# Performance work log

Measured on AMD Instinct MI355X. Metric: run time of the kernel, lower is better.

The kernel has to match this reference:

```python
import jax, jax.numpy as jnp
import numpy as np

B, S, D, K, N = 4, 4096, 768, 24, 8192

def setup_inputs() -> dict:
    key = jax.random.key(0)
    k1, k2, k3, k4 = jax.random.split(key, 4)
    x = jax.random.normal(k1, (B, S, D), dtype=jnp.float32)
    phi = jax.random.normal(k2, (S, K), dtype=jnp.float32)
    M_inputs = jax.random.normal(k3, (D, D), dtype=jnp.float32) / np.sqrt(D)
    M_filters = jax.random.normal(k4, (K, D), dtype=jnp.float32) / np.sqrt(K)
    return {"x": x, "phi": phi, "M_inputs": M_inputs, "M_filters": M_filters, "n": N}


def reference(x, phi, M_inputs, M_filters, n):
    # STU.forward with use_approx=True, use_flash_fft=False
    bsz, sl, d = x.shape
    x_proj = x @ M_inputs               # [B, S, D]
    phi_proj = phi @ M_filters          # [S, D]
    # alternating sign sequence for the 'minus' spectral branch
    sgn = jnp.ones((1, sl, 1), dtype=x.dtype).at[:, 1::2].set(-1.0)
    # filters: [1, S, D, 1] broadcast over the plus/minus stack
    v = phi_proj[None, :, :, None]
    V = jnp.fft.rfft(v, n=n, axis=1)    # [1, n//2+1, D, 1] complex
    U = jnp.stack([x_proj, x_proj * sgn], axis=-1)  # [B, S, D, 2]
    Uf = jnp.fft.rfft(U, n=n, axis=1)   # [B, n//2+1, D, 2]
    U_conv = jnp.fft.irfft(V * Uf, n=n, axis=1)[:, :sl]  # [B, S, D, 2]
    spectral_plus = U_conv[..., 0]
    spectral_minus = U_conv[..., 1] * sgn
    return spectral_plus + spectral_minus
```

## Files before the change

kernel.cpp:

```cpp
#include <hip/hip_runtime.h>
#include <hip/hip_bf16.h>


#define NB 4
#define NS 4096
#define ND 768
#define NK 24

typedef __attribute__((ext_vector_type(8))) short short8;
typedef __attribute__((ext_vector_type(4))) float f32x4;
typedef __attribute__((ext_vector_type(4))) unsigned short u16x4;

static __device__ __forceinline__ float bf2f(unsigned short u) {
  union { unsigned int i; float f; } v; v.i = ((unsigned int)u) << 16; return v.f;
}
static __device__ __forceinline__ unsigned short f2bf(float f) {
  union { float f; unsigned int i; } v; v.f = f;
  return (unsigned short)((v.i + 0x7fffu + ((v.i >> 16) & 1u)) >> 16);
}

__device__ __forceinline__ float2 cadd(float2 a, float2 b){ return make_float2(a.x+b.x, a.y+b.y); }
__device__ __forceinline__ float2 csub(float2 a, float2 b){ return make_float2(a.x-b.x, a.y-b.y); }
__device__ __forceinline__ float2 cmul(float2 a, float2 b){ return make_float2(a.x*b.x-a.y*b.y, a.x*b.y+a.y*b.x); }

#define C4 0.70710678118654752f
#define C8 0.92387953251128674f
#define S8 0.38268343236508977f
#define TWO_PI 6.28318530717958648f

__device__ __forceinline__ void fft16_dif(float2 v[16]) {
  const float twr[8] = {1.f, C8, C4, S8, 0.f, -S8, -C4, -C8};
  const float twi[8] = {0.f, -S8, -C4, -C8, -1.f, -C8, -C4, -S8};
#pragma unroll
  for (int i = 0; i < 8; ++i) {
    float2 a = v[i], b = v[i+8];
    v[i] = cadd(a, b);
    float2 d = csub(a, b);
    v[i+8] = make_float2(d.x*twr[i]-d.y*twi[i], d.x*twi[i]+d.y*twr[i]);
  }
#pragma unroll
  for (int blk = 0; blk < 16; blk += 8)
#pragma unroll
    for (int i = 0; i < 4; ++i) {
      float2 a = v[blk+i], b = v[blk+i+4];
      v[blk+i] = cadd(a, b);
      float2 d = csub(a, b);
      v[blk+i+4] = make_float2(d.x*twr[2*i]-d.y*twi[2*i], d.x*twi[2*i]+d.y*twr[2*i]);
    }
#pragma unroll
  for (int blk = 0; blk < 16; blk += 4) {
    { float2 a = v[blk],   b = v[blk+2]; v[blk] = cadd(a,b);   v[blk+2] = csub(a,b); }
    { float2 a = v[blk+1], b = v[blk+3]; float2 d = csub(a,b);
      v[blk+1] = cadd(a,b); v[blk+3] = make_float2(d.y, -d.x); }
  }
#pragma unroll
  for (int blk = 0; blk < 16; blk += 2) {
    float2 a = v[blk], b = v[blk+1];
    v[blk] = cadd(a, b); v[blk+1] = csub(a, b);
  }
}

__device__ __forceinline__ void idft16(float2 v[16]) {
  const float twr[8] = {1.f, C8, C4, S8, 0.f, -S8, -C4, -C8};
  const float twi[8] = {0.f, S8, C4, C8, 1.f, C8, C4, S8};
#pragma unroll
  for (int blk = 0; blk < 16; blk += 2) {
    float2 a = v[blk], b = v[blk+1];
    v[blk] = cadd(a, b); v[blk+1] = csub(a, b);
  }
#pragma unroll
  for (int blk = 0; blk < 16; blk += 4) {
    { float2 a = v[blk],   b = v[blk+2]; v[blk] = cadd(a,b);   v[blk+2] = csub(a,b); }
    { float2 a = v[blk+1], b = v[blk+3]; float2 t = make_float2(-b.y, b.x);
      v[blk+1] = cadd(a,t); v[blk+3] = csub(a,t); }
  }
#pragma unroll
  for (int blk = 0; blk < 16; blk += 8)
#pragma unroll
    for (int i = 0; i < 4; ++i) {
      float2 b = v[blk+i+4];
      float2 t = make_float2(b.x*twr[2*i]-b.y*twi[2*i], b.x*twi[2*i]+b.y*twr[2*i]);
      float2 a = v[blk+i];
      v[blk+i] = cadd(a, t); v[blk+i+4] = csub(a, t);
    }
#pragma unroll
  for (int i = 0; i < 8; ++i) {
    float2 b = v[i+8];
    float2 t = make_float2(b.x*twr[i]-b.y*twi[i], b.x*twi[i]+b.y*twr[i]);
    float2 a = v[i];
    v[i] = cadd(a, t); v[i+8] = csub(a, t);
  }
}

#define BR_TABLE {0,8,4,12,2,10,6,14,1,9,5,13,3,11,7,15}
#define PAD(i) ((i) + ((i) >> 4))

__global__ __launch_bounds__(256) void cast_x_bf16(const float* __restrict__ in,
                                                   unsigned short* __restrict__ out) {
  int i = (blockIdx.x * 256 + threadIdx.x) * 4;
  float4 v = *(const float4*)(in + i);
  u16x4 o = { f2bf(v.x), f2bf(v.y), f2bf(v.z), f2bf(v.w) };
  *(u16x4*)(out + i) = o;
}

__global__ __launch_bounds__(256) void transpose_cast_Mi(const float* __restrict__ Mi,
                                                         unsigned short* __restrict__ MiT) {
  int idx = blockIdx.x * 256 + threadIdx.x;
  int d = idx / ND, e = idx % ND;
  MiT[idx] = f2bf(Mi[e * ND + d]);
}

__global__ __launch_bounds__(256) void phi_proj_kernel(const float* __restrict__ phi,
                                                       const float* __restrict__ Mf,
                                                       float* __restrict__ phiE) {
  int d = blockIdx.y;
  int m = blockIdx.x * 256 + threadIdx.x;
  int s = 2 * m;
  float acc = 0.f;
#pragma unroll
  for (int k = 0; k < NK; ++k) acc += phi[s * NK + k] * Mf[k * ND + d];
  phiE[d * 2048 + m] = acc;
}

__global__ __launch_bounds__(256) void gemm_xprojT(const unsigned short* __restrict__ Xb,
                                                   const unsigned short* __restrict__ MiT,
                                                   unsigned short* __restrict__ XPT) {
  __shared__ unsigned short As[128 * 32];
  __shared__ unsigned short Bs[128 * 32];
  const int tid = threadIdx.x;
  const int r0 = blockIdx.x * 128;
  const int c0 = blockIdx.y * 128;
  const int lane = tid & 63;
  const int wave = tid >> 6;
  const int wr = (wave >> 1) * 64;
  const int wc = (wave & 1) * 64;

  f32x4 acc[4][4];
#pragma unroll
  for (int m = 0; m < 4; ++m)
#pragma unroll
    for (int n = 0; n < 4; ++n) acc[m][n] = (f32x4){0.f, 0.f, 0.f, 0.f};

  for (int k0 = 0; k0 < ND; k0 += 32) {
    short8 va[2], vb[2];
#pragma unroll
    for (int i = 0; i < 2; ++i) {
      int slot = tid + 256 * i;
      int row = slot >> 2, kc = slot & 3;
      va[i] = *(const short8*)(Xb + (size_t)(r0 + row) * ND + k0 + kc * 8);
      vb[i] = *(const short8*)(MiT + (size_t)(c0 + row) * ND + k0 + kc * 8);
    }
    __syncthreads();
#pragma unroll
    for (int i = 0; i < 2; ++i) {
      int slot = tid + 256 * i;
      *(short8*)(As + slot * 8) = va[i];
      *(short8*)(Bs + slot * 8) = vb[i];
    }
    __syncthreads();

    short8 a[4], b[4];
#pragma unroll
    for (int m = 0; m < 4; ++m)
      a[m] = *(const short8*)(As + (wr + m * 16 + (lane & 15)) * 32 + (lane >> 4) * 8);
#pragma unroll
    for (int n = 0; n < 4; ++n)
      b[n] = *(const short8*)(Bs + (wc + n * 16 + (lane & 15)) * 32 + (lane >> 4) * 8);
#pragma unroll
    for (int m = 0; m < 4; ++m)
#pragma unroll
      for (int n = 0; n < 4; ++n)
        acc[m][n] = __builtin_amdgcn_mfma_f32_16x16x32_bf16(a[m], b[n], acc[m][n], 0, 0, 0);
  }

  const int bI = r0 >> 12;
  const int sBase = r0 & (NS - 1);
#pragma unroll
  for (int m = 0; m < 4; ++m) {
#pragma unroll
    for (int n = 0; n < 4; ++n) {
      int col = c0 + wc + n * 16 + (lane & 15);
      int srow = sBase + wr + m * 16 + (lane >> 4) * 4;
      f32x4 v = acc[m][n];
      u16x4 o = { f2bf(v[0]), f2bf(v[1]), f2bf(v[2]), f2bf(v[3]) };
      *(u16x4*)(XPT + ((size_t)bI * ND + col) * NS + srow) = o;
    }
  }
}

__global__ __launch_bounds__(256) void filter_fft(const float* __restrict__ phiE,
                                                  float2* __restrict__ Hbr) {
  __shared__ float LR[4352], LI[4352];
  const int d = blockIdx.x;
  const int tid = threadIdx.x;
  const int BR[16] = BR_TABLE;
  float2 v[16];
  const float* src = phiE + (size_t)d * 2048;
#pragma unroll
  for (int n2 = 0; n2 < 16; ++n2)
    v[n2] = (n2 < 8) ? make_float2(src[n2 * 256 + tid], 0.f) : make_float2(0.f, 0.f);

  float sn, cs;
  fft16_dif(v);
  __sincosf(-(TWO_PI / 4096.f) * (float)tid, &sn, &cs);
  { float2 step = make_float2(cs, sn), w = make_float2(1.f, 0.f);
#pragma unroll
    for (int p = 1; p < 16; ++p) { w = cmul(w, step); v[BR[p]] = cmul(v[BR[p]], w); } }
#pragma unroll
  for (int r = 0; r < 16; ++r) { int i = BR[r] * 256 + tid; int s = PAD(i); LR[s] = v[r].x; LI[s] = v[r].y; }
  __syncthreads();

  const int p2 = tid >> 4, n0 = tid & 15;
#pragma unroll
  for (int n1 = 0; n1 < 16; ++n1) { int i = p2 * 256 + n1 * 16 + n0; int s = PAD(i); v[n1] = make_float2(LR[s], LI[s]); }
  fft16_dif(v);
  __sincosf(-(TWO_PI / 256.f) * (float)n0, &sn, &cs);
  { float2 step = make_float2(cs, sn), w = make_float2(1.f, 0.f);
#pragma unroll
    for (int p = 1; p < 16; ++p) { w = cmul(w, step); v[BR[p]] = cmul(v[BR[p]], w); } }
  __syncthreads();
#pragma unroll
  for (int r = 0; r < 16; ++r) { int i = p2 * 256 + BR[r] * 16 + n0; int s = PAD(i); LR[s] = v[r].x; LI[s] = v[r].y; }
  __syncthreads();

#pragma unroll
  for (int q = 0; q < 16; ++q) { int i = tid * 16 + q; int s = PAD(i); v[q] = make_float2(LR[s], LI[s]); }
  fft16_dif(v);
  const float sc = 2.0f / 4096.0f;
  float2* H = Hbr + (size_t)d * 4096;
#pragma unroll
  for (int r = 0; r < 16; ++r)
    H[r * 256 + tid] = make_float2(v[r].x * sc, v[r].y * sc);
}

__global__ __launch_bounds__(256) void conv_kernel(const unsigned short* __restrict__ XPT,
                                                   const float2* __restrict__ Hbr,
                                                   float* __restrict__ outT) {
  __shared__ float LR[4352], LI[4352];
  const int bd = blockIdx.x;
  const int d = bd % ND;
  const int tid = threadIdx.x;
  const int BR[16] = BR_TABLE;
  float2 v[16];
  float sn, cs;

  const unsigned int* src = (const unsigned int*)(XPT + (size_t)bd * NS);
#pragma unroll
  for (int n2 = 0; n2 < 16; ++n2) {
    if (n2 < 8) {
      unsigned int w = src[n2 * 256 + tid];
      v[n2] = make_float2(bf2f((unsigned short)(w & 0xffffu)), bf2f((unsigned short)(w >> 16)));
    } else v[n2] = make_float2(0.f, 0.f);
  }

  fft16_dif(v);
  __sincosf(-(TWO_PI / 4096.f) * (float)tid, &sn, &cs);
  { float2 step = make_float2(cs, sn), w = make_float2(1.f, 0.f);
#pragma unroll
    for (int p = 1; p < 16; ++p) { w = cmul(w, step); v[BR[p]] = cmul(v[BR[p]], w); } }
#pragma unroll
  for (int r = 0; r < 16; ++r) { int i = BR[r] * 256 + tid; int s = PAD(i); LR[s] = v[r].x; LI[s] = v[r].y; }
  __syncthreads();

  const int p2 = tid >> 4, n0 = tid & 15;
#pragma unroll
  for (int n1 = 0; n1 < 16; ++n1) { int i = p2 * 256 + n1 * 16 + n0; int s = PAD(i); v[n1] = make_float2(LR[s], LI[s]); }
  fft16_dif(v);
  __sincosf(-(TWO_PI / 256.f) * (float)n0, &sn, &cs);
  { float2 step = make_float2(cs, sn), w = make_float2(1.f, 0.f);
#pragma unroll
    for (int p = 1; p < 16; ++p) { w = cmul(w, step); v[BR[p]] = cmul(v[BR[p]], w); } }
  __syncthreads();
#pragma unroll
  for (int r = 0; r < 16; ++r) { int i = p2 * 256 + BR[r] * 16 + n0; int s = PAD(i); LR[s] = v[r].x; LI[s] = v[r].y; }
  __syncthreads();

#pragma unroll
  for (int q = 0; q < 16; ++q) { int i = tid * 16 + q; int s = PAD(i); v[q] = make_float2(LR[s], LI[s]); }
  fft16_dif(v);
  const float2* H = Hbr + (size_t)d * 4096;
#pragma unroll
  for (int r = 0; r < 16; ++r) v[r] = cmul(v[r], H[r * 256 + tid]);
  idft16(v);
  __sincosf((TWO_PI / 256.f) * (float)(tid & 15), &sn, &cs);
  { float2 step = make_float2(cs, sn), w = make_float2(1.f, 0.f);
#pragma unroll
    for (int n = 1; n < 16; ++n) { w = cmul(w, step); v[n] = cmul(v[n], w); } }
#pragma unroll
  for (int n = 0; n < 16; ++n) { int i = tid * 16 + n; int s = PAD(i); LR[s] = v[n].x; LI[s] = v[n].y; }
  __syncthreads();

#pragma unroll
  for (int r = 0; r < 16; ++r) { int i = p2 * 256 + BR[r] * 16 + n0; int s = PAD(i); v[r] = make_float2(LR[s], LI[s]); }
  idft16(v);
  {
    float sn0, cs0;
    __sincosf((TWO_PI / 4096.f) * (float)(n0 * p2), &sn0, &cs0);
    __sincosf((TWO_PI / 256.f) * (float)p2, &sn, &cs);
    float2 step = make_float2(cs, sn), w = make_float2(cs0, sn0);
    v[0] = cmul(v[0], w);
#pragma unroll
    for (int n = 1; n < 16; ++n) { w = cmul(w, step); v[n] = cmul(v[n], w); }
  }
  __syncthreads();
#pragma unroll
  for (int n = 0; n < 16; ++n) { int i = p2 * 256 + n * 16 + n0; int s = PAD(i); LR[s] = v[n].x; LI[s] = v[n].y; }
  __syncthreads();

#pragma unroll
  for (int r = 0; r < 16; ++r) { int i = BR[r] * 256 + tid; int s = PAD(i); v[r] = make_float2(LR[s], LI[s]); }
  idft16(v);
  float* dst = outT + (size_t)bd * NS;
#pragma unroll
  for (int n2 = 0; n2 < 8; ++n2)
    *(float2*)(dst + ((n2 << 8) + tid) * 2) = v[n2];
}

__global__ __launch_bounds__(256) void transpose_out(const float* __restrict__ outT,
                                                     float* __restrict__ out) {
  __shared__ float tile[64][65];
  const int b = blockIdx.z;
  const int d0 = blockIdx.y * 64;
  const int s0 = blockIdx.x * 64;
  const int tid = threadIdx.x;
#pragma unroll
  for (int i = 0; i < 16; ++i) {
    int dd = (tid >> 6) + i * 4;
    int ss = tid & 63;
    tile[dd][ss] = outT[((size_t)b * ND + d0 + dd) * NS + s0 + ss];
  }
  __syncthreads();
#pragma unroll
  for (int i = 0; i < 16; ++i) {
    int ss = (tid >> 6) + i * 4;
    int dd = tid & 63;
    out[((size_t)b * NS + s0 + ss) * ND + d0 + dd] = tile[dd][ss];
  }
}

extern "C" void kernel_launch(void* const* d_in, const int* in_sizes, int n_in,
                              void* d_out, int out_size, void* d_ws, size_t ws_size,
                              hipStream_t stream) {
  const float* x   = (const float*)d_in[0];
  const float* phi = (const float*)d_in[1];
  const float* Mi  = (const float*)d_in[2];
  const float* Mf  = (const float*)d_in[3];
  float* out = (float*)d_out;

  const size_t SZ_XPT = (size_t)NB * ND * NS * 2;
  const size_t SZ_HBR = (size_t)ND * 4096 * 8;
  const size_t SZ_POOL = (size_t)NB * ND * NS * 4;
  if (ws_size < SZ_XPT + SZ_HBR + SZ_POOL) return;

  char* ws = (char*)d_ws;
  unsigned short* xprojT = (unsigned short*)ws;
  float2* Hbr = (float2*)(ws + SZ_XPT);
  char* pool = ws + SZ_XPT + SZ_HBR;
  unsigned short* xbf = (unsigned short*)pool;
  unsigned short* MiT = (unsigned short*)(pool + 25165824);
  float* phiE = (float*)(pool + 25165824 + 1179648);
  float* outT = (float*)pool;

  cast_x_bf16<<<(NB * NS * ND) / (256 * 4), 256, 0, stream>>>(x, xbf);
  transpose_cast_Mi<<<(ND * ND) / 256, 256, 0, stream>>>(Mi, MiT);
  phi_proj_kernel<<<dim3(2048 / 256, ND), 256, 0, stream>>>(phi, Mf, phiE);
  gemm_xprojT<<<dim3((NB * NS) / 128, ND / 128), 256, 0, stream>>>(xbf, MiT, xprojT);
  filter_fft<<<ND, 256, 0, stream>>>(phiE, Hbr);
  conv_kernel<<<NB * ND, 256, 0, stream>>>(xprojT, Hbr, outT);
  transpose_out<<<dim3(NS / 64, ND / 64, NB), 256, 0, stream>>>(outT, out);
}
```

Measured before the change: 136.7 us.

## Table twiddles, prune zero-padded FFT stages, bf16 intermediate, direct-to-LDS GEMM loads

Bundles several changes. A precomputed twiddle table replaces per-thread sincos and chained complex multiplies. Specialised FFT stages skip the zero-padded half on input and the unused half on output. The phi projection is fused into filter_fft, the Mi transpose is tiled through LDS, and the GEMM uses global_load_lds with a swapped grid order. The conv output is stored as bf16 to halve transpose traffic, at the cost of extra rounding error in the final result.

Result: slower. 175.1 us (+28.1%).

```diff
diff --git a/kernel.cpp b/kernel.cpp
--- a/kernel.cpp
+++ b/kernel.cpp
@@ -22,6 +22,7 @@
 __device__ __forceinline__ float2 cadd(float2 a, float2 b){ return make_float2(a.x+b.x, a.y+b.y); }
 __device__ __forceinline__ float2 csub(float2 a, float2 b){ return make_float2(a.x-b.x, a.y-b.y); }
 __device__ __forceinline__ float2 cmul(float2 a, float2 b){ return make_float2(a.x*b.x-a.y*b.y, a.x*b.y+a.y*b.x); }
+__device__ __forceinline__ float2 cmulc(float2 a, float2 b){ return make_float2(a.x*b.x+a.y*b.y, a.y*b.x-a.x*b.y); }
 
 #define C4 0.70710678118654752f
 #define C8 0.92387953251128674f
@@ -60,6 +61,37 @@
   }
 }
 
+__device__ __forceinline__ void fft16_dif_zero8(float2 v[16]) {
+  const float twr[8] = {1.f, C8, C4, S8, 0.f, -S8, -C4, -C8};
+  const float twi[8] = {0.f, -S8, -C4, -C8, -1.f, -C8, -C4, -S8};
+#pragma unroll
+  for (int i = 1; i < 8; ++i) {
+    float2 a = v[i];
+    v[i+8] = make_float2(a.x*twr[i]-a.y*twi[i], a.x*twi[i]+a.y*twr[i]);
+  }
+  v[8] = v[0];
+#pragma unroll
+  for (int blk = 0; blk < 16; blk += 8)
+#pragma unroll
+    for (int i = 0; i < 4; ++i) {
+      float2 a = v[blk+i], b = v[blk+i+4];
+      v[blk+i] = cadd(a, b);
+      float2 d = csub(a, b);
+      v[blk+i+4] = make_float2(d.x*twr[2*i]-d.y*twi[2*i], d.x*twi[2*i]+d.y*twr[2*i]);
+    }
+#pragma unroll
+  for (int blk = 0; blk < 16; blk += 4) {
+    { float2 a = v[blk],   b = v[blk+2]; v[blk] = cadd(a,b);   v[blk+2] = csub(a,b); }
+    { float2 a = v[blk+1], b = v[blk+3]; float2 d = csub(a,b);
+      v[blk+1] = cadd(a,b); v[blk+3] = make_float2(d.y, -d.x); }
+  }
+#pragma unroll
+  for (int blk = 0; blk < 16; blk += 2) {
+    float2 a = v[blk], b = v[blk+1];
+    v[blk] = cadd(a, b); v[blk+1] = csub(a, b);
+  }
+}
+
 __device__ __forceinline__ void idft16(float2 v[16]) {
   const float twr[8] = {1.f, C8, C4, S8, 0.f, -S8, -C4, -C8};
   const float twi[8] = {0.f, S8, C4, C8, 1.f, C8, C4, S8};
@@ -92,8 +124,48 @@
   }
 }
 
+__device__ __forceinline__ void idft16_low8(float2 v[16]) {
+  const float twr[8] = {1.f, C8, C4, S8, 0.f, -S8, -C4, -C8};
+  const float twi[8] = {0.f, S8, C4, C8, 1.f, C8, C4, S8};
+#pragma unroll
+  for (int blk = 0; blk < 16; blk += 2) {
+    float2 a = v[blk], b = v[blk+1];
+    v[blk] = cadd(a, b); v[blk+1] = csub(a, b);
+  }
+#pragma unroll
+  for (int blk = 0; blk < 16; blk += 4) {
+    { float2 a = v[blk],   b = v[blk+2]; v[blk] = cadd(a,b);   v[blk+2] = csub(a,b); }
+    { float2 a = v[blk+1], b = v[blk+3]; float2 t = make_float2(-b.y, b.x);
+      v[blk+1] = cadd(a,t); v[blk+3] = csub(a,t); }
+  }
+#pragma unroll
+  for (int blk = 0; blk < 16; blk += 8)
+#pragma unroll
+    for (int i = 0; i < 4; ++i) {
+      float2 b = v[blk+i+4];
+      float2 t = make_float2(b.x*twr[2*i]-b.y*twi[2*i], b.x*twi[2*i]+b.y*twr[2*i]);
+      float2 a = v[blk+i];
+      v[blk+i] = cadd(a, t); v[blk+i+4] = csub(a, t);
+    }
+#pragma unroll
+  for (int i = 0; i < 8; ++i) {
+    float2 b = v[i+8];
+    float2 t = make_float2(b.x*twr[i]-b.y*twi[i], b.x*twi[i]+b.y*twr[i]);
+    v[i] = cadd(v[i], t);
+  }
+}
+
 #define BR_TABLE {0,8,4,12,2,10,6,14,1,9,5,13,3,11,7,15}
 #define PAD(i) ((i) + ((i) >> 4))
+
+__global__ __launch_bounds__(256) void twiddle_init(float2* __restrict__ T1) {
+  int idx = blockIdx.x * 256 + threadIdx.x;
+  int p = idx >> 8, t = idx & 255;
+  float ang = -(TWO_PI / 4096.f) * (float)(p * t);
+  float sn, cs;
+  __sincosf(ang, &sn, &cs);
+  T1[idx] = make_float2(cs, sn);
+}
 
 __global__ __launch_bounds__(256) void cast_x_bf16(const float* __restrict__ in,
                                                    unsigned short* __restrict__ out) {
@@ -105,21 +177,25 @@
 
 __global__ __launch_bounds__(256) void transpose_cast_Mi(const float* __restrict__ Mi,
                                                          unsigned short* __restrict__ MiT) {
-  int idx = blockIdx.x * 256 + threadIdx.x;
-  int d = idx / ND, e = idx % ND;
-  MiT[idx] = f2bf(Mi[e * ND + d]);
-}
-
-__global__ __launch_bounds__(256) void phi_proj_kernel(const float* __restrict__ phi,
-                                                       const float* __restrict__ Mf,
-                                                       float* __restrict__ phiE) {
-  int d = blockIdx.y;
-  int m = blockIdx.x * 256 + threadIdx.x;
-  int s = 2 * m;
-  float acc = 0.f;
-#pragma unroll
-  for (int k = 0; k < NK; ++k) acc += phi[s * NK + k] * Mf[k * ND + d];
-  phiE[d * 2048 + m] = acc;
+  __shared__ float tile[64][65];
+  const int d0 = blockIdx.x * 64;
+  const int e0 = blockIdx.y * 64;
+  const int tid = threadIdx.x;
+#pragma unroll
+  for (int i = 0; i < 16; ++i) {
+    int ee = (tid >> 6) + i * 4;
+    int dd = tid & 63;
+    tile[ee][dd] = Mi[(e0 + ee) * ND + d0 + dd];
+  }
+  __syncthreads();
+#pragma unroll
+  for (int i = 0; i < 8; ++i) {
+    int dd = (tid >> 5) + i * 8;
+    int ee2 = (tid & 31) * 2;
+    unsigned int w = (unsigned int)f2bf(tile[ee2][dd]) |
+                     ((unsigned int)f2bf(tile[ee2 + 1][dd]) << 16);
+    *(unsigned int*)(MiT + (size_t)(d0 + dd) * ND + e0 + ee2) = w;
+  }
 }
 
 __global__ __launch_bounds__(256) void gemm_xprojT(const unsigned short* __restrict__ Xb,
@@ -128,10 +204,10 @@
   __shared__ unsigned short As[128 * 32];
   __shared__ unsigned short Bs[128 * 32];
   const int tid = threadIdx.x;
-  const int r0 = blockIdx.x * 128;
-  const int c0 = blockIdx.y * 128;
   const int lane = tid & 63;
   const int wave = tid >> 6;
+  const int c0 = blockIdx.x * 128;
+  const int r0 = blockIdx.y * 128;
   const int wr = (wave >> 1) * 64;
   const int wc = (wave & 1) * 64;
 
@@ -141,21 +217,23 @@
 #pragma unroll
     for (int n = 0; n < 4; ++n) acc[m][n] = (f32x4){0.f, 0.f, 0.f, 0.f};
 
+  const int ldRow = (lane >> 2);
+  const int ldK = (lane & 3) * 8;
+
   for (int k0 = 0; k0 < ND; k0 += 32) {
-    short8 va[2], vb[2];
-#pragma unroll
-    for (int i = 0; i < 2; ++i) {
-      int slot = tid + 256 * i;
-      int row = slot >> 2, kc = slot & 3;
-      va[i] = *(const short8*)(Xb + (size_t)(r0 + row) * ND + k0 + kc * 8);
-      vb[i] = *(const short8*)(MiT + (size_t)(c0 + row) * ND + k0 + kc * 8);
-    }
-    __syncthreads();
-#pragma unroll
-    for (int i = 0; i < 2; ++i) {
-      int slot = tid + 256 * i;
-      *(short8*)(As + slot * 8) = va[i];
-      *(short8*)(Bs + slot * 8) = vb[i];
+    if (k0) __syncthreads();
+#pragma unroll
+    for (int h = 0; h < 2; ++h) {
+      int c = wave * 2 + h;
+      int row = c * 16 + ldRow;
+      const unsigned short* ga = Xb + (size_t)(r0 + row) * ND + k0 + ldK;
+      const unsigned short* gb = MiT + (size_t)(c0 + row) * ND + k0 + ldK;
+      __builtin_amdgcn_global_load_lds(
+          (const __attribute__((address_space(1))) void*)ga,
+          (__attribute__((address_space(3))) void*)(As + c * 512), 16, 0, 0);
+      __builtin_amdgcn_global_load_lds(
+          (const __attribute__((address_space(1))) void*)gb,
+          (__attribute__((address_space(3))) void*)(Bs + c * 512), 16, 0, 0);
     }
     __syncthreads();
 
@@ -188,24 +266,34 @@
   }
 }
 
-__global__ __launch_bounds__(256) void filter_fft(const float* __restrict__ phiE,
+__global__ __launch_bounds__(256) void filter_fft(const float* __restrict__ phi,
+                                                  const float* __restrict__ Mf,
+                                                  const float2* __restrict__ T1,
                                                   float2* __restrict__ Hbr) {
   __shared__ float LR[4352], LI[4352];
   const int d = blockIdx.x;
   const int tid = threadIdx.x;
   const int BR[16] = BR_TABLE;
   float2 v[16];
-  const float* src = phiE + (size_t)d * 2048;
-#pragma unroll
-  for (int n2 = 0; n2 < 16; ++n2)
-    v[n2] = (n2 < 8) ? make_float2(src[n2 * 256 + tid], 0.f) : make_float2(0.f, 0.f);
-
-  float sn, cs;
-  fft16_dif(v);
-  __sincosf(-(TWO_PI / 4096.f) * (float)tid, &sn, &cs);
-  { float2 step = make_float2(cs, sn), w = make_float2(1.f, 0.f);
-#pragma unroll
-    for (int p = 1; p < 16; ++p) { w = cmul(w, step); v[BR[p]] = cmul(v[BR[p]], w); } }
+
+  float mf[NK];
+#pragma unroll
+  for (int k = 0; k < NK; ++k) mf[k] = Mf[k * ND + d];
+#pragma unroll
+  for (int n2 = 0; n2 < 8; ++n2) {
+    int m = n2 * 256 + tid;
+    const float* pr = phi + (size_t)(2 * m) * NK;
+    float acc = 0.f;
+#pragma unroll
+    for (int k = 0; k < NK; ++k) acc += pr[k] * mf[k];
+    v[n2] = make_float2(acc, 0.f);
+  }
+#pragma unroll
+  for (int n2 = 8; n2 < 16; ++n2) v[n2] = make_float2(0.f, 0.f);
+
+  fft16_dif_zero8(v);
+#pragma unroll
+  for (int p = 1; p < 16; ++p) v[BR[p]] = cmul(v[BR[p]], T1[p * 256 + tid]);
 #pragma unroll
   for (int r = 0; r < 16; ++r) { int i = BR[r] * 256 + tid; int s = PAD(i); LR[s] = v[r].x; LI[s] = v[r].y; }
   __syncthreads();
@@ -214,10 +302,8 @@
 #pragma unroll
   for (int n1 = 0; n1 < 16; ++n1) { int i = p2 * 256 + n1 * 16 + n0; int s = PAD(i); v[n1] = make_float2(LR[s], LI[s]); }
   fft16_dif(v);
-  __sincosf(-(TWO_PI / 256.f) * (float)n0, &sn, &cs);
-  { float2 step = make_float2(cs, sn), w = make_float2(1.f, 0.f);
-#pragma unroll
-    for (int p = 1; p < 16; ++p) { w = cmul(w, step); v[BR[p]] = cmul(v[BR[p]], w); } }
+#pragma unroll
+  for (int p = 1; p < 16; ++p) v[BR[p]] = cmul(v[BR[p]], T1[p * 256 + 16 * n0]);
   __syncthreads();
 #pragma unroll
   for (int r = 0; r < 16; ++r) { int i = p2 * 256 + BR[r] * 16 + n0; int s = PAD(i); LR[s] = v[r].x; LI[s] = v[r].y; }
@@ -235,29 +321,27 @@
 
 __global__ __launch_bounds__(256) void conv_kernel(const unsigned short* __restrict__ XPT,
                                                    const float2* __restrict__ Hbr,
-                                                   float* __restrict__ outT) {
+                                                   const float2* __restrict__ T1,
+                                                   unsigned int* __restrict__ outTb) {
   __shared__ float LR[4352], LI[4352];
   const int bd = blockIdx.x;
   const int d = bd % ND;
   const int tid = threadIdx.x;
   const int BR[16] = BR_TABLE;
   float2 v[16];
-  float sn, cs;
 
   const unsigned int* src = (const unsigned int*)(XPT + (size_t)bd * NS);
 #pragma unroll
-  for (int n2 = 0; n2 < 16; ++n2) {
-    if (n2 < 8) {
-      unsigned int w = src[n2 * 256 + tid];
-      v[n2] = make_float2(bf2f((unsigned short)(w & 0xffffu)), bf2f((unsigned short)(w >> 16)));
-    } else v[n2] = make_float2(0.f, 0.f);
-  }
-
-  fft16_dif(v);
-  __sincosf(-(TWO_PI / 4096.f) * (float)tid, &sn, &cs);
-  { float2 step = make_float2(cs, sn), w = make_float2(1.f, 0.f);
-#pragma unroll
-    for (int p = 1; p < 16; ++p) { w = cmul(w, step); v[BR[p]] = cmul(v[BR[p]], w); } }
+  for (int n2 = 0; n2 < 8; ++n2) {
+    unsigned int w = src[n2 * 256 + tid];
+    v[n2] = make_float2(bf2f((unsigned short)(w & 0xffffu)), bf2f((unsigned short)(w >> 16)));
+  }
+#pragma unroll
+  for (int n2 = 8; n2 < 16; ++n2) v[n2] = make_float2(0.f, 0.f);
+
+  fft16_dif_zero8(v);
+#pragma unroll
+  for (int p = 1; p < 16; ++p) v[BR[p]] = cmul(v[BR[p]], T1[p * 256 + tid]);
 #pragma unroll
   for (int r = 0; r < 16; ++r) { int i = BR[r] * 256 + tid; int s = PAD(i); LR[s] = v[r].x; LI[s] = v[r].y; }
   __syncthreads();
@@ -266,10 +350,8 @@
 #pragma unroll
   for (int n1 = 0; n1 < 16; ++n1) { int i = p2 * 256 + n1 * 16 + n0; int s = PAD(i); v[n1] = make_float2(LR[s], LI[s]); }
   fft16_dif(v);
-  __sincosf(-(TWO_PI / 256.f) * (float)n0, &sn, &cs);
-  { float2 step = make_float2(cs, sn), w = make_float2(1.f, 0.f);
-#pragma unroll
-    for (int p = 1; p < 16; ++p) { w = cmul(w, step); v[BR[p]] = cmul(v[BR[p]], w); } }
+#pragma unroll
+  for (int p = 1; p < 16; ++p) v[BR[p]] = cmul(v[BR[p]], T1[p * 256 + 16 * n0]);
   __syncthreads();
 #pragma unroll
   for (int r = 0; r < 16; ++r) { int i = p2 * 256 + BR[r] * 16 + n0; int s = PAD(i); LR[s] = v[r].x; LI[s] = v[r].y; }
@@ -282,10 +364,8 @@
 #pragma unroll
   for (int r = 0; r < 16; ++r) v[r] = cmul(v[r], H[r * 256 + tid]);
   idft16(v);
-  __sincosf((TWO_PI / 256.f) * (float)(tid & 15), &sn, &cs);
-  { float2 step = make_float2(cs, sn), w = make_float2(1.f, 0.f);
-#pragma unroll
-    for (int n = 1; n < 16; ++n) { w = cmul(w, step); v[n] = cmul(v[n], w); } }
+#pragma unroll
+  for (int n = 1; n < 16; ++n) v[n] = cmulc(v[n], T1[n * 256 + 16 * (tid & 15)]);
 #pragma unroll
   for (int n = 0; n < 16; ++n) { int i = tid * 16 + n; int s = PAD(i); LR[s] = v[n].x; LI[s] = v[n].y; }
   __syncthreads();
@@ -293,15 +373,8 @@
 #pragma unroll
   for (int r = 0; r < 16; ++r) { int i = p2 * 256 + BR[r] * 16 + n0; int s = PAD(i); v[r] = make_float2(LR[s], LI[s]); }
   idft16(v);
-  {
-    float sn0, cs0;
-    __sincosf((TWO_PI / 4096.f) * (float)(n0 * p2), &sn0, &cs0);
-    __sincosf((TWO_PI / 256.f) * (float)p2, &sn, &cs);
-    float2 step = make_float2(cs, sn), w = make_float2(cs0, sn0);
-    v[0] = cmul(v[0], w);
-#pragma unroll
-    for (int n = 1; n < 16; ++n) { w = cmul(w, step); v[n] = cmul(v[n], w); }
-  }
+#pragma unroll
+  for (int n = 0; n < 16; ++n) v[n] = cmulc(v[n], T1[p2 * 256 + 16 * n + n0]);
   __syncthreads();
 #pragma unroll
   for (int n = 0; n < 16; ++n) { int i = p2 * 256 + n * 16 + n0; int s = PAD(i); LR[s] = v[n].x; LI[s] = v[n].y; }
@@ -309,14 +382,17 @@
 
 #pragma unroll
   for (int r = 0; r < 16; ++r) { int i = BR[r] * 256 + tid; int s = PAD(i); v[r] = make_float2(LR[s], LI[s]); }
-  idft16(v);
-  float* dst = outT + (size_t)bd * NS;
-#pragma unroll
-  for (int n2 = 0; n2 < 8; ++n2)
-    *(float2*)(dst + ((n2 << 8) + tid) * 2) = v[n2];
-}
-
-__global__ __launch_bounds__(256) void transpose_out(const float* __restrict__ outT,
+  idft16_low8(v);
+  unsigned int* dst = outTb + (size_t)bd * 2048;
+#pragma unroll
+  for (int n2 = 0; n2 < 8; ++n2) {
+    float2 y = v[n2];
+    unsigned int w = (unsigned int)f2bf(y.x) | ((unsigned int)f2bf(y.y) << 16);
+    dst[(n2 << 8) + tid] = w;
+  }
+}
+
+__global__ __launch_bounds__(256) void transpose_out(const unsigned int* __restrict__ outTb,
                                                      float* __restrict__ out) {
   __shared__ float tile[64][65];
   const int b = blockIdx.z;
@@ -324,10 +400,12 @@
   const int s0 = blockIdx.x * 64;
   const int tid = threadIdx.x;
 #pragma unroll
-  for (int i = 0; i < 16; ++i) {
-    int dd = (tid >> 6) + i * 4;
-    int ss = tid & 63;
-    tile[dd][ss] = outT[((size_t)b * ND + d0 + dd) * NS + s0 + ss];
+  for (int i = 0; i < 8; ++i) {
+    int dd = (tid >> 5) + i * 8;
+    int ss2 = (tid & 31) * 2;
+    unsigned int w = outTb[(((size_t)b * ND + d0 + dd) * NS + s0 + ss2) >> 1];
+    tile[dd][ss2]     = bf2f((unsigned short)(w & 0xffffu));
+    tile[dd][ss2 + 1] = bf2f((unsigned short)(w >> 16));
   }
   __syncthreads();
 #pragma unroll
@@ -357,15 +435,15 @@
   float2* Hbr = (float2*)(ws + SZ_XPT);
   char* pool = ws + SZ_XPT + SZ_HBR;
   unsigned short* xbf = (unsigned short*)pool;
+  unsigned int* outTb = (unsigned int*)pool;
   unsigned short* MiT = (unsigned short*)(pool + 25165824);
-  float* phiE = (float*)(pool + 25165824 + 1179648);
-  float* outT = (float*)pool;
+  float2* T1 = (float2*)(pool + 25165824 + 2097152);
 
   cast_x_bf16<<<(NB * NS * ND) / (256 * 4), 256, 0, stream>>>(x, xbf);
-  transpose_cast_Mi<<<(ND * ND) / 256, 256, 0, stream>>>(Mi, MiT);
-  phi_proj_kernel<<<dim3(2048 / 256, ND), 256, 0, stream>>>(phi, Mf, phiE);
-  gemm_xprojT<<<dim3((NB * NS) / 128, ND / 128), 256, 0, stream>>>(xbf, MiT, xprojT);
-  filter_fft<<<ND, 256, 0, stream>>>(phiE, Hbr);
-  conv_kernel<<<NB * ND, 256, 0, stream>>>(xprojT, Hbr, outT);
-  transpose_out<<<dim3(NS / 64, ND / 64, NB), 256, 0, stream>>>(outT, out);
-}
+  transpose_cast_Mi<<<dim3(ND / 64, ND / 64), 256, 0, stream>>>(Mi, MiT);
+  twiddle_init<<<16, 256, 0, stream>>>(T1);
+  gemm_xprojT<<<dim3(ND / 128, (NB * NS) / 128), 256, 0, stream>>>(xbf, MiT, xprojT);
+  filter_fft<<<ND, 256, 0, stream>>>(phi, Mf, T1, Hbr);
+  conv_kernel<<<NB * ND, 256, 0, stream>>>(xprojT, Hbr, T1, outTb);
+  transpose_out<<<dim3(NS / 64, ND / 64, NB), 256, 0, stream>>>(outTb, out);
+}
```
